# Kernel optimization log

Measured on AMD Instinct MI355X. Metric: run time of the kernel, lower is better.

The kernel has to match this reference:

```python
import jax, jax.numpy as jnp
import numpy as np

B, H, W, C = 8, 64, 64, 512
SCALING = 8
C_ = C // SCALING  # 64
N = H * W          # 4096


def setup_inputs() -> dict:
    key = jax.random.key(0)
    ks = jax.random.split(key, 8)
    scale = 1.0 / np.sqrt(C)
    x = jax.random.normal(ks[0], (B, H, W, C), dtype=jnp.float32)
    # 1x1 convs == per-pixel dense layers: weight [C_in, C_out] + bias
    Wg = jax.random.normal(ks[1], (C, C_), dtype=jnp.float32) * scale
    bg = jnp.zeros((C_,), dtype=jnp.float32)
    Wf = jax.random.normal(ks[2], (C, C_), dtype=jnp.float32) * scale
    bf = jnp.zeros((C_,), dtype=jnp.float32)
    Wh = jax.random.normal(ks[3], (C, C), dtype=jnp.float32) * scale
    bh = jnp.zeros((C,), dtype=jnp.float32)
    gamma = jnp.zeros((C,), dtype=jnp.float32)  # tf.initializers.Zeros
    return {"x": x, "Wg": Wg, "bg": bg, "Wf": Wf, "bf": bf,
            "Wh": Wh, "bh": bh, "gamma": gamma}


def reference(x, Wg, bg, Wf, bf, Wh, bh, gamma):
    b = x.shape[0]
    xf_flat = x.reshape(b, N, C)                     # [B, N, C]
    x_g = xf_flat @ Wg + bg                          # [B, N, C_]
    x_f = xf_flat @ Wf + bf                          # [B, N, C_]
    x_h = xf_flat @ Wh + bh                          # [B, N, C]
    s = jnp.einsum('bnc,bmc->bnm', x_g, x_f)         # [B, N, N]
    s = jax.nn.softmax(s, axis=-1)
    o = jnp.einsum('bnm,bmc->bnc', s, x_h)           # [B, N, C]
    o = o.reshape(b, H, W, C)
    return gamma * o + x
```

## Files before the change

### kernel.cpp

```cpp
#include <hip/hip_runtime.h>
#include <stdint.h>

using s8v  = __attribute__((ext_vector_type(8))) short;
using f4   = __attribute__((ext_vector_type(4))) float;
using u32x4 = __attribute__((ext_vector_type(4))) uint32_t;
using u32x2 = __attribute__((ext_vector_type(2))) uint32_t;
using vf4  = __attribute__((ext_vector_type(4))) float;
using i4v  = __attribute__((ext_vector_type(4))) int;

typedef unsigned short ushortT;

#define LOG2E 1.4426950408889634f

static __device__ __forceinline__ uint32_t bfr16(float f) {
  union { float f; uint32_t u; } v; v.f = f;
  return (v.u + 0x7FFFu + ((v.u >> 16) & 1u)) >> 16;
}
static __device__ __forceinline__ uint32_t pk2(float lo, float hi) {
  return (bfr16(hi) << 16) | (bfr16(lo) & 0xFFFFu);
}
static __device__ __forceinline__ uint32_t pk4fp8(float a, float b, float cc, float d) {
  int w = __builtin_amdgcn_cvt_pk_fp8_f32(a, b, 0, false);
  w = __builtin_amdgcn_cvt_pk_fp8_f32(cc, d, w, true);
  return (uint32_t)w;
}
static __device__ __forceinline__ float ex2(float x) {
#if __has_builtin(__builtin_amdgcn_exp2f)
  return __builtin_amdgcn_exp2f(x);
#else
  float r; asm("v_exp_f32 %0, %1" : "=v"(r) : "v"(x)); return r;
#endif
}
static __device__ __forceinline__ void gl16(const void* g, void* l) {
  __builtin_amdgcn_global_load_lds((const __attribute__((address_space(1))) uint32_t*)g,
                                   (__attribute__((address_space(3))) uint32_t*)l, 16, 0, 0);
}

#define MFMA_BF16(A, B, C) __builtin_amdgcn_mfma_f32_16x16x32_bf16((A), (B), (C), 0, 0, 0)
#define MFMA_FP8(A, B, C)  __builtin_amdgcn_mfma_f32_16x16x32_fp8_fp8((A), (B), (C), 0, 0, 0)

__global__ __launch_bounds__(64) void kprep(const float* __restrict__ Wg,
                                            const float* __restrict__ Wf,
                                            const float* __restrict__ Wh,
                                            ushortT* __restrict__ Wt) {
  const int cIdx = blockIdx.x;
  const int t = threadIdx.x;
  const float* src; int co, ldc;
  if (cIdx < 64)       { src = Wg; co = cIdx;       ldc = 64;  }
  else if (cIdx < 128) { src = Wf; co = cIdx - 64;  ldc = 64;  }
  else                 { src = Wh; co = cIdx - 128; ldc = 512; }
#pragma unroll
  for (int kk = 0; kk < 8; ++kk) {
    int k = kk * 64 + t;
    Wt[(size_t)cIdx * 512 + k] = (ushortT)bfr16(src[(size_t)k * ldc + co]);
  }
}

__global__ __launch_bounds__(256) void kproj(const float* __restrict__ x,
                                             const ushortT* __restrict__ Wt,
                                             const float* __restrict__ bg,
                                             const float* __restrict__ bfv,
                                             const float* __restrict__ bh,
                                             ushortT* __restrict__ Q,
                                             ushortT* __restrict__ K,
                                             uint8_t* __restrict__ V8) {
  __shared__ ushortT Al[128 * 64];
  __shared__ ushortT Bl[128 * 64];

  const int tid = threadIdx.x;
  const int w = tid >> 6, l = tid & 63, h = l >> 4, c = l & 15;
  const int wr = w >> 1, wc = w & 1;
  const int ct = blockIdx.x, rt = blockIdx.y;
  const int row0 = rt * 128;

  f4 acc[4][4];
#pragma unroll
  for (int m = 0; m < 4; ++m)
#pragma unroll
    for (int n = 0; n < 4; ++n) acc[m][n] = (f4){0.f, 0.f, 0.f, 0.f};

  const int arow = tid >> 1, ahalf = tid & 1;
  const float* xrow = x + (size_t)(row0 + arow) * 512 + ahalf * 32;
  const int asw = arow & 7;

  for (int kk = 0; kk < 8; ++kk) {
    const int k0 = kk * 64;
    vf4 f[8];
#pragma unroll
    for (int i = 0; i < 8; ++i) f[i] = *(const vf4*)(xrow + k0 + i * 4);
#pragma unroll
    for (int j = 0; j < 4; ++j) {
      u32x4 ch = { pk2(f[2*j][0], f[2*j][1]),   pk2(f[2*j][2], f[2*j][3]),
                   pk2(f[2*j+1][0], f[2*j+1][1]), pk2(f[2*j+1][2], f[2*j+1][3]) };
      *(u32x4*)((char*)Al + arow * 128 + (((ahalf * 4 + j) ^ asw) * 16)) = ch;
    }
#pragma unroll
    for (int i = 0; i < 4; ++i) {
      const int col = w * 32 + i * 8 + (l >> 3);
      const ushortT* src = Wt + (size_t)(ct * 128 + col) * 512 + k0 +
                           8 * ((l & 7) ^ (l >> 3));
      gl16(src, (char*)Bl + (w * 4 + i) * 1024);
    }
    __syncthreads();
#pragma unroll
    for (int ks = 0; ks < 2; ++ks) {
      s8v a[4], b[4];
#pragma unroll
      for (int m = 0; m < 4; ++m)
        a[m] = *(const s8v*)((char*)Al + (size_t)(wr * 64 + m * 16 + c) * 128 +
                             (((ks * 4 + h) ^ (c & 7)) * 16));
#pragma unroll
      for (int n = 0; n < 4; ++n)
        b[n] = *(const s8v*)((char*)Bl + (size_t)(wc * 64 + n * 16 + c) * 128 +
                             (((ks * 4 + h) ^ (c & 7)) * 16));
#pragma unroll
      for (int m = 0; m < 4; ++m)
#pragma unroll
        for (int n = 0; n < 4; ++n)
          acc[m][n] = MFMA_BF16(a[m], b[n], acc[m][n]);
    }
    __syncthreads();
  }

  if (ct == 0) {
    ushortT* dst = (wc == 0) ? Q : K;
    const float* bias = (wc == 0) ? bg : bfv;
    const float scl = (wc == 0) ? LOG2E : 1.0f;
#pragma unroll
    for (int n = 0; n < 4; ++n) {
      const int col = n * 16 + c;
      const float bv = bias[col];
#pragma unroll
      for (int m = 0; m < 4; ++m) {
        const int grow = row0 + wr * 64 + m * 16 + h * 4;
#pragma unroll
        for (int r = 0; r < 4; ++r)
          dst[(size_t)(grow + r) * 64 + col] = (ushortT)bfr16((acc[m][n][r] + bv) * scl);
      }
    }
  } else {
    const int b = row0 >> 12;
#pragma unroll
    for (int n = 0; n < 4; ++n) {
      const int vcol = ct * 128 + wc * 64 + n * 16 + c - 128;
      const float bv = bh[vcol];
#pragma unroll
      for (int m = 0; m < 4; ++m) {
        const int n0 = (row0 & 4095) + wr * 64 + m * 16 + h * 4;
        const int tt = n0 >> 5, kvo = n0 & 31;
        const uint32_t dd = pk4fp8(acc[m][n][0] + bv, acc[m][n][1] + bv,
                                   acc[m][n][2] + bv, acc[m][n][3] + bv);
        *(uint32_t*)(V8 + (((size_t)(b * 128 + tt) * 512 + vcol) * 32 + kvo)) = dd;
      }
    }
  }
}

__global__ __launch_bounds__(512, 4) void kattn(const ushortT* __restrict__ Qg,
                                                const ushortT* __restrict__ Kg,
                                                const uint8_t* __restrict__ V8,
                                                const float* __restrict__ x,
                                                const float* __restrict__ gamma,
                                                float* __restrict__ out) {
  __shared__ __align__(16) uint32_t Pl[2][2][512];
  __shared__ __align__(16) ushortT Klds[2][64 * 64];
  __shared__ __align__(16) float alpha_s[2][64];
  __shared__ __align__(16) int   flag_s[2][4];
  __shared__ __align__(16) float lsum_s[64];

  const int tid = threadIdx.x;
  const int w = tid >> 6, l = tid & 63, h = l >> 4, c = l & 15;
  const int bb = blockIdx.x & 7, qb = blockIdx.x >> 3;
  const size_t qrow0 = (size_t)bb * 4096 + (size_t)qb * 64;

  f4 acc[4][4];
#pragma unroll
  for (int qi = 0; qi < 4; ++qi)
#pragma unroll
    for (int vj = 0; vj < 4; ++vj) acc[qi][vj] = (f4){0.f, 0.f, 0.f, 0.f};

  const ushortT* Kb = Kg + (size_t)bb * 4096 * 64;
  const uint8_t* Vb = V8 + (size_t)bb * 512 * 4096;

  const uint8_t* vptr = Vb + (size_t)(w * 64 + c) * 32 + h * 8;
  const size_t koff = (size_t)((w & 3) * 16 + (l >> 3)) * 64 +
                      8 * ((l & 7) ^ (l >> 3));

  s8v qf[2];
  if (w < 4) {
#pragma unroll
    for (int ks = 0; ks < 2; ++ks)
      qf[ks] = *(const s8v*)(Qg + (qrow0 + w * 16 + c) * 64 + ks * 32 + h * 8);
  }
  float m_run = -__builtin_inff();
  float l_run = 0.0f;

  auto softmax_store = [&](const f4* sc, int nb) {
    float tm = fmaxf(fmaxf(fmaxf(sc[0][0], sc[0][1]), fmaxf(sc[0][2], sc[0][3])),
                     fmaxf(fmaxf(sc[1][0], sc[1][1]), fmaxf(sc[1][2], sc[1][3])));
    tm = fmaxf(tm, fmaxf(fmaxf(fmaxf(sc[2][0], sc[2][1]), fmaxf(sc[2][2], sc[2][3])),
                         fmaxf(fmaxf(sc[3][0], sc[3][1]), fmaxf(sc[3][2], sc[3][3]))));
    const unsigned long long bal = __ballot(tm > m_run + 5.77f);
    float al = 1.0f;
    if (bal) {
      tm = fmaxf(tm, __shfl_xor(tm, 16));
      tm = fmaxf(tm, __shfl_xor(tm, 32));
      const float mn = fmaxf(m_run, tm);
      al = ex2(m_run - mn);
      m_run = mn;
    }
    float ps = 0.0f;
#pragma unroll
    for (int j = 0; j < 4; ++j) {
      const float p0 = ex2(sc[j][0] - m_run), p1 = ex2(sc[j][1] - m_run);
      const float p2 = ex2(sc[j][2] - m_run), p3 = ex2(sc[j][3] - m_run);
      ps += (p0 + p1) + (p2 + p3);
      const uint32_t pw = pk4fp8(p0, p1, p2, p3);
      const int s = j >> 1;
      const int hc = 2 * (j & 1) + (h >> 1);
      Pl[nb][s][(w * 64 + c + 16 * hc) * 2 + (h & 1)] = pw;
    }
    l_run = l_run * al + ps;
    if (bal && h == 0) alpha_s[nb][w * 16 + c] = al;
    if (l == 0) flag_s[nb][w] = bal ? 1 : 0;
  };

  auto produce_lds = [&](int kb, int nb) {
    f4 sc[4];
#pragma unroll
    for (int j = 0; j < 4; ++j) sc[j] = (f4){0.f, 0.f, 0.f, 0.f};
    const char* kbp = (const char*)Klds[kb];
    __builtin_amdgcn_s_setprio(1);
#pragma unroll
    for (int j = 0; j < 4; ++j) {
#pragma unroll
      for (int ks = 0; ks < 2; ++ks) {
        s8v kf = *(const s8v*)(kbp + (size_t)(j * 16 + c) * 128 +
                               (((ks * 4 + h) ^ (c & 7)) * 16));
        sc[j] = MFMA_BF16(kf, qf[ks], sc[j]);
      }
    }
    __builtin_amdgcn_s_setprio(0);
    softmax_store(sc, nb);
  };

  if (w < 4) {
    f4 sc[4];
#pragma unroll
    for (int j = 0; j < 4; ++j) sc[j] = (f4){0.f, 0.f, 0.f, 0.f};
#pragma unroll
    for (int j = 0; j < 4; ++j) {
#pragma unroll
      for (int ks = 0; ks < 2; ++ks) {
        s8v kf = *(const s8v*)(Kb + (size_t)(j * 16 + c) * 64 + ks * 32 + h * 8);
        sc[j] = MFMA_BF16(kf, qf[ks], sc[j]);
      }
    }
    softmax_store(sc, 0);
  } else {
    gl16(Kb + 4096 + koff, (char*)Klds[1] + (w & 3) * 2048);
    gl16(Kb + 4096 + koff + 512, (char*)Klds[1] + (w & 3) * 2048 + 1024);
  }
  asm volatile("s_waitcnt vmcnt(0) lgkmcnt(0)" ::: "memory");
  __builtin_amdgcn_s_barrier();

  for (int t = 0; t < 64; ++t) {
    const int cur = t & 1;
    long paA[4], paB[4];
#pragma unroll
    for (int qi = 0; qi < 4; ++qi) {
      paA[qi] = *(const long*)&Pl[cur][0][(qi * 64 + l) * 2];
      paB[qi] = *(const long*)&Pl[cur][1][(qi * 64 + l) * 2];
    }
    i4v fl = *(const i4v*)&flag_s[cur][0];
    if (w >= 4 && t < 62) {
      const ushortT* ks_src = Kb + (size_t)(t + 2) * 4096 + koff;
      gl16(ks_src, (char*)Klds[cur] + (w & 3) * 2048);
      gl16(ks_src + 512, (char*)Klds[cur] + (w & 3) * 2048 + 1024);
    }
#pragma unroll
    for (int qi = 0; qi < 4; ++qi) {
      if (fl[qi]) {
        f4 a4 = *(const f4*)&alpha_s[cur][qi * 16 + h * 4];
#pragma unroll
        for (int vj = 0; vj < 4; ++vj)
#pragma unroll
          for (int r = 0; r < 4; ++r) acc[qi][vj][r] *= a4[r];
      }
    }
#pragma unroll
    for (int vj = 0; vj < 4; ++vj) {
      const long vf0 = *(const long*)(vptr + vj * 512);
      const long vf1 = *(const long*)(vptr + 16384 + vj * 512);
      __builtin_amdgcn_s_setprio(1);
#pragma unroll
      for (int qi = 0; qi < 4; ++qi) {
        acc[qi][vj] = MFMA_FP8(paA[qi], vf0, acc[qi][vj]);
        acc[qi][vj] = MFMA_FP8(paB[qi], vf1, acc[qi][vj]);
      }
      __builtin_amdgcn_s_setprio(0);
    }
    vptr += 32768;
    if (t < 63) {
      if (w < 4) produce_lds(cur ^ 1, cur ^ 1);
      asm volatile("s_waitcnt vmcnt(0) lgkmcnt(0)" ::: "memory");
      __builtin_amdgcn_s_barrier();
    }
  }

  l_run += __shfl_xor(l_run, 16);
  l_run += __shfl_xor(l_run, 32);
  if (w < 4 && h == 0) lsum_s[w * 16 + c] = l_run;
  __syncthreads();
#pragma unroll
  for (int qi = 0; qi < 4; ++qi) {
    f4 l4 = *(const f4*)(&lsum_s[qi * 16 + h * 4]);
    f4 rl;
#pragma unroll
    for (int r = 0; r < 4; ++r) rl[r] = 1.0f / l4[r];
#pragma unroll
    for (int vj = 0; vj < 4; ++vj) {
      const int colg = w * 64 + vj * 16 + c;
      const float gm = gamma[colg];
#pragma unroll
      for (int r = 0; r < 4; ++r) {
        const size_t idx = (qrow0 + qi * 16 + h * 4 + r) * 512 + colg;
        out[idx] = gm * (acc[qi][vj][r] * rl[r]) + x[idx];
      }
    }
  }
}

extern "C" void kernel_launch(void* const* d_in, const int* in_sizes, int n_in,
                              void* d_out, int out_size, void* d_ws, size_t ws_size,
                              hipStream_t stream) {
  const float* x     = (const float*)d_in[0];
  const float* Wg    = (const float*)d_in[1];
  const float* bg    = (const float*)d_in[2];
  const float* Wf    = (const float*)d_in[3];
  const float* bfv   = (const float*)d_in[4];
  const float* Wh    = (const float*)d_in[5];
  const float* bh    = (const float*)d_in[6];
  const float* gamma = (const float*)d_in[7];
  float* out = (float*)d_out;
  char* ws = (char*)d_ws;

  ushortT* Q  = (ushortT*)(ws);
  ushortT* K  = (ushortT*)(ws + ((size_t)4 << 20));
  uint8_t* V8 = (uint8_t*)(ws + ((size_t)8 << 20));
  ushortT* Wt = (ushortT*)(ws + ((size_t)40 << 20));

  kprep<<<dim3(640), dim3(64), 0, stream>>>(Wg, Wf, Wh, Wt);
  kproj<<<dim3(5, 256), dim3(256), 0, stream>>>(x, Wt, bg, bfv, bh, Q, K, V8);
  kattn<<<dim3(512), dim3(512), 0, stream>>>(Q, K, V8, x, gamma, out);
}
```

Measured before the change: 235.8 us.

## Use MX-scaled 16x16x128 fp8 MFMA with 128-key tiles and bf16 pre-converted x

The attention loop now handles 128 keys per step, so there are half as many barriers and pipeline stages. The P·V product uses the scaled f8f6f4 16x16x128 MFMA with unit scales in place of pairs of 16x16x32 fp8 MFMAs, with P and V laid out to feed 32-byte fragments. A separate kernel converts x to bf16 once, storing it in the output buffer as scratch, so the projection kernel can fill shared memory with direct global-to-LDS loads. The costs are an extra kernel launch with its own memory pass, doubled K LDS buffers, and higher register pressure in the attention kernel.

```diff
diff --git a/kernel.cpp b/kernel.cpp
--- a/kernel.cpp
+++ b/kernel.cpp
@@ -3,6 +3,7 @@
 
 using s8v  = __attribute__((ext_vector_type(8))) short;
 using f4   = __attribute__((ext_vector_type(4))) float;
+using i8v  = __attribute__((ext_vector_type(8))) int;
 using u32x4 = __attribute__((ext_vector_type(4))) uint32_t;
 using u32x2 = __attribute__((ext_vector_type(2))) uint32_t;
 using vf4  = __attribute__((ext_vector_type(4))) float;
@@ -37,7 +38,24 @@
 }
 
 #define MFMA_BF16(A, B, C) __builtin_amdgcn_mfma_f32_16x16x32_bf16((A), (B), (C), 0, 0, 0)
-#define MFMA_FP8(A, B, C)  __builtin_amdgcn_mfma_f32_16x16x32_fp8_fp8((A), (B), (C), 0, 0, 0)
+#define MFMA_MX(A, B, C) \
+  __builtin_amdgcn_mfma_scale_f32_16x16x128_f8f6f4((A), (B), (C), 0, 0, \
+                                                   0, 0x7F7F7F7F, 0, 0x7F7F7F7F)
+
+__global__ __launch_bounds__(256) void kxcvt(const float* __restrict__ x,
+                                             ushortT* __restrict__ xb) {
+  const size_t stride = (size_t)2048 * 256 * 8;
+  size_t idx = ((size_t)blockIdx.x * 256 + threadIdx.x) * 8;
+#pragma unroll
+  for (int i = 0; i < 4; ++i) {
+    vf4 a = *(const vf4*)(x + idx);
+    vf4 b = *(const vf4*)(x + idx + 4);
+    u32x4 o = { pk2(a[0], a[1]), pk2(a[2], a[3]),
+                pk2(b[0], b[1]), pk2(b[2], b[3]) };
+    *(u32x4*)(xb + idx) = o;
+    idx += stride;
+  }
+}
 
 __global__ __launch_bounds__(64) void kprep(const float* __restrict__ Wg,
                                             const float* __restrict__ Wf,
@@ -56,7 +74,7 @@
   }
 }
 
-__global__ __launch_bounds__(256) void kproj(const float* __restrict__ x,
+__global__ __launch_bounds__(256) void kproj(const ushortT* __restrict__ xb,
                                              const ushortT* __restrict__ Wt,
                                              const float* __restrict__ bg,
                                              const float* __restrict__ bfv,
@@ -79,20 +97,15 @@
 #pragma unroll
     for (int n = 0; n < 4; ++n) acc[m][n] = (f4){0.f, 0.f, 0.f, 0.f};
 
-  const int arow = tid >> 1, ahalf = tid & 1;
-  const float* xrow = x + (size_t)(row0 + arow) * 512 + ahalf * 32;
-  const int asw = arow & 7;
-
   for (int kk = 0; kk < 8; ++kk) {
     const int k0 = kk * 64;
-    vf4 f[8];
-#pragma unroll
-    for (int i = 0; i < 8; ++i) f[i] = *(const vf4*)(xrow + k0 + i * 4);
-#pragma unroll
-    for (int j = 0; j < 4; ++j) {
-      u32x4 ch = { pk2(f[2*j][0], f[2*j][1]),   pk2(f[2*j][2], f[2*j][3]),
-                   pk2(f[2*j+1][0], f[2*j+1][1]), pk2(f[2*j+1][2], f[2*j+1][3]) };
-      *(u32x4*)((char*)Al + arow * 128 + (((ahalf * 4 + j) ^ asw) * 16)) = ch;
+#pragma unroll
+    for (int i = 0; i < 4; ++i) {
+      const int ch = i * 256 + tid;
+      const int row = ch >> 3, kc = ch & 7;
+      const ushortT* src = xb + (size_t)(row0 + row) * 512 + k0 +
+                           8 * (kc ^ (row & 7));
+      gl16(src, (char*)Al + ch * 16);
     }
 #pragma unroll
     for (int i = 0; i < 4; ++i) {
@@ -162,8 +175,8 @@
                                                 const float* __restrict__ x,
                                                 const float* __restrict__ gamma,
                                                 float* __restrict__ out) {
-  __shared__ __align__(16) uint32_t Pl[2][2][512];
-  __shared__ __align__(16) ushortT Klds[2][64 * 64];
+  __shared__ __align__(16) uint32_t Pl[2][2048];
+  __shared__ __align__(16) ushortT Klds[2][2][64 * 64];
   __shared__ __align__(16) float alpha_s[2][64];
   __shared__ __align__(16) int   flag_s[2][4];
   __shared__ __align__(16) float lsum_s[64];
@@ -182,7 +195,7 @@
   const ushortT* Kb = Kg + (size_t)bb * 4096 * 64;
   const uint8_t* Vb = V8 + (size_t)bb * 512 * 4096;
 
-  const uint8_t* vptr = Vb + (size_t)(w * 64 + c) * 32 + h * 8;
+  const uint8_t* vptr = Vb + (size_t)h * 16384 + (size_t)(w * 64 + c) * 32;
   const size_t koff = (size_t)((w & 3) * 16 + (l >> 3)) * 64 +
                       8 * ((l & 7) ^ (l >> 3));
 
@@ -195,11 +208,12 @@
   float m_run = -__builtin_inff();
   float l_run = 0.0f;
 
-  auto softmax_store = [&](const f4* sc, int nb) {
-    float tm = fmaxf(fmaxf(fmaxf(sc[0][0], sc[0][1]), fmaxf(sc[0][2], sc[0][3])),
-                     fmaxf(fmaxf(sc[1][0], sc[1][1]), fmaxf(sc[1][2], sc[1][3])));
-    tm = fmaxf(tm, fmaxf(fmaxf(fmaxf(sc[2][0], sc[2][1]), fmaxf(sc[2][2], sc[2][3])),
-                         fmaxf(fmaxf(sc[3][0], sc[3][1]), fmaxf(sc[3][2], sc[3][3]))));
+  auto softmax_store8 = [&](const f4* sc, int nb) {
+    float tm = sc[0][0];
+#pragma unroll
+    for (int idx = 0; idx < 8; ++idx)
+#pragma unroll
+      for (int r = 0; r < 4; ++r) tm = fmaxf(tm, sc[idx][r]);
     const unsigned long long bal = __ballot(tm > m_run + 5.77f);
     float al = 1.0f;
     if (bal) {
@@ -211,72 +225,80 @@
     }
     float ps = 0.0f;
 #pragma unroll
-    for (int j = 0; j < 4; ++j) {
-      const float p0 = ex2(sc[j][0] - m_run), p1 = ex2(sc[j][1] - m_run);
-      const float p2 = ex2(sc[j][2] - m_run), p3 = ex2(sc[j][3] - m_run);
-      ps += (p0 + p1) + (p2 + p3);
-      const uint32_t pw = pk4fp8(p0, p1, p2, p3);
-      const int s = j >> 1;
-      const int hc = 2 * (j & 1) + (h >> 1);
-      Pl[nb][s][(w * 64 + c + 16 * hc) * 2 + (h & 1)] = pw;
-    }
+    for (int T = 0; T < 2; ++T)
+#pragma unroll
+      for (int j = 0; j < 4; ++j) {
+        const int idx = T * 4 + j;
+        const float p0 = ex2(sc[idx][0] - m_run), p1 = ex2(sc[idx][1] - m_run);
+        const float p2 = ex2(sc[idx][2] - m_run), p3 = ex2(sc[idx][3] - m_run);
+        ps += (p0 + p1) + (p2 + p3);
+        const uint32_t pw = pk4fp8(p0, p1, p2, p3);
+        Pl[nb][(w * 64 + c + 16 * (2 * T + (j >> 1))) * 8 + 4 * (j & 1) + h] = pw;
+      }
     l_run = l_run * al + ps;
     if (bal && h == 0) alpha_s[nb][w * 16 + c] = al;
     if (l == 0) flag_s[nb][w] = bal ? 1 : 0;
   };
 
   auto produce_lds = [&](int kb, int nb) {
-    f4 sc[4];
-#pragma unroll
-    for (int j = 0; j < 4; ++j) sc[j] = (f4){0.f, 0.f, 0.f, 0.f};
-    const char* kbp = (const char*)Klds[kb];
+    f4 sc[8];
+#pragma unroll
+    for (int i = 0; i < 8; ++i) sc[i] = (f4){0.f, 0.f, 0.f, 0.f};
     __builtin_amdgcn_s_setprio(1);
 #pragma unroll
-    for (int j = 0; j < 4; ++j) {
-#pragma unroll
-      for (int ks = 0; ks < 2; ++ks) {
-        s8v kf = *(const s8v*)(kbp + (size_t)(j * 16 + c) * 128 +
-                               (((ks * 4 + h) ^ (c & 7)) * 16));
-        sc[j] = MFMA_BF16(kf, qf[ks], sc[j]);
-      }
+    for (int T = 0; T < 2; ++T) {
+      const char* kbp = (const char*)Klds[kb][T];
+#pragma unroll
+      for (int j = 0; j < 4; ++j)
+#pragma unroll
+        for (int ks = 0; ks < 2; ++ks) {
+          s8v kf = *(const s8v*)(kbp + (size_t)(j * 16 + c) * 128 +
+                                 (((ks * 4 + h) ^ (c & 7)) * 16));
+          sc[T * 4 + j] = MFMA_BF16(kf, qf[ks], sc[T * 4 + j]);
+        }
     }
     __builtin_amdgcn_s_setprio(0);
-    softmax_store(sc, nb);
+    softmax_store8(sc, nb);
   };
 
   if (w < 4) {
-    f4 sc[4];
-#pragma unroll
-    for (int j = 0; j < 4; ++j) sc[j] = (f4){0.f, 0.f, 0.f, 0.f};
-#pragma unroll
-    for (int j = 0; j < 4; ++j) {
-#pragma unroll
-      for (int ks = 0; ks < 2; ++ks) {
-        s8v kf = *(const s8v*)(Kb + (size_t)(j * 16 + c) * 64 + ks * 32 + h * 8);
-        sc[j] = MFMA_BF16(kf, qf[ks], sc[j]);
-      }
-    }
-    softmax_store(sc, 0);
+    f4 sc[8];
+#pragma unroll
+    for (int i = 0; i < 8; ++i) sc[i] = (f4){0.f, 0.f, 0.f, 0.f};
+#pragma unroll
+    for (int T = 0; T < 2; ++T)
+#pragma unroll
+      for (int j = 0; j < 4; ++j)
+#pragma unroll
+        for (int ks = 0; ks < 2; ++ks) {
+          s8v kf = *(const s8v*)(Kb + (size_t)(T * 64 + j * 16 + c) * 64 +
+                                 ks * 32 + h * 8);
+          sc[T * 4 + j] = MFMA_BF16(kf, qf[ks], sc[T * 4 + j]);
+        }
+    softmax_store8(sc, 0);
   } else {
-    gl16(Kb + 4096 + koff, (char*)Klds[1] + (w & 3) * 2048);
-    gl16(Kb + 4096 + koff + 512, (char*)Klds[1] + (w & 3) * 2048 + 1024);
+    const ushortT* ksrc = Kb + 8192 + koff;
+    gl16(ksrc,              (char*)Klds[1][0] + (w & 3) * 2048);
+    gl16(ksrc + 512,        (char*)Klds[1][0] + (w & 3) * 2048 + 1024);
+    gl16(ksrc + 4096,       (char*)Klds[1][1] + (w & 3) * 2048);
+    gl16(ksrc + 4096 + 512, (char*)Klds[1][1] + (w & 3) * 2048 + 1024);
   }
   asm volatile("s_waitcnt vmcnt(0) lgkmcnt(0)" ::: "memory");
   __builtin_amdgcn_s_barrier();
 
-  for (int t = 0; t < 64; ++t) {
-    const int cur = t & 1;
-    long paA[4], paB[4];
-#pragma unroll
-    for (int qi = 0; qi < 4; ++qi) {
-      paA[qi] = *(const long*)&Pl[cur][0][(qi * 64 + l) * 2];
-      paB[qi] = *(const long*)&Pl[cur][1][(qi * 64 + l) * 2];
-    }
+  for (int e = 0; e < 32; ++e) {
+    const int cur = e & 1;
+    i8v pa[4];
+#pragma unroll
+    for (int qi = 0; qi < 4; ++qi)
+      pa[qi] = *(const i8v*)&Pl[cur][(qi * 64 + l) * 8];
     i4v fl = *(const i4v*)&flag_s[cur][0];
-    if (w >= 4 && t < 62) {
-      const ushortT* ks_src = Kb + (size_t)(t + 2) * 4096 + koff;
-      gl16(ks_src, (char*)Klds[cur] + (w & 3) * 2048);
-      gl16(ks_src + 512, (char*)Klds[cur] + (w & 3) * 2048 + 1024);
+    if (w >= 4 && e < 30) {
+      const ushortT* ksrc = Kb + (size_t)(e + 2) * 8192 + koff;
+      gl16(ksrc,              (char*)Klds[cur][0] + (w & 3) * 2048);
+      gl16(ksrc + 512,        (char*)Klds[cur][0] + (w & 3) * 2048 + 1024);
+      gl16(ksrc + 4096,       (char*)Klds[cur][1] + (w & 3) * 2048);
+      gl16(ksrc + 4096 + 512, (char*)Klds[cur][1] + (w & 3) * 2048 + 1024);
     }
 #pragma unroll
     for (int qi = 0; qi < 4; ++qi) {
@@ -290,19 +312,16 @@
     }
 #pragma unroll
     for (int vj = 0; vj < 4; ++vj) {
-      const long vf0 = *(const long*)(vptr + vj * 512);
-      const long vf1 = *(const long*)(vptr + 16384 + vj * 512);
+      const i8v vf = *(const i8v*)(vptr + vj * 512);
       __builtin_amdgcn_s_setprio(1);
 #pragma unroll
-      for (int qi = 0; qi < 4; ++qi) {
-        acc[qi][vj] = MFMA_FP8(paA[qi], vf0, acc[qi][vj]);
-        acc[qi][vj] = MFMA_FP8(paB[qi], vf1, acc[qi][vj]);
-      }
+      for (int qi = 0; qi < 4; ++qi)
+        acc[qi][vj] = MFMA_MX(pa[qi], vf, acc[qi][vj]);
       __builtin_amdgcn_s_setprio(0);
     }
-    vptr += 32768;
-    if (t < 63) {
-      if (w < 4) produce_lds(cur ^ 1, cur ^ 1);
+    vptr += 65536;
+    if (w < 4 && e < 31) produce_lds(cur ^ 1, cur ^ 1);
+    if (e < 31) {
       asm volatile("s_waitcnt vmcnt(0) lgkmcnt(0)" ::: "memory");
       __builtin_amdgcn_s_barrier();
     }
@@ -349,8 +368,10 @@
   ushortT* K  = (ushortT*)(ws + ((size_t)4 << 20));
   uint8_t* V8 = (uint8_t*)(ws + ((size_t)8 << 20));
   ushortT* Wt = (ushortT*)(ws + ((size_t)40 << 20));
-
+  ushortT* xb = (ushortT*)d_out;
+
+  kxcvt<<<dim3(2048), dim3(256), 0, stream>>>(x, xb);
   kprep<<<dim3(640), dim3(64), 0, stream>>>(Wg, Wf, Wh, Wt);
-  kproj<<<dim3(5, 256), dim3(256), 0, stream>>>(x, Wt, bg, bfv, bh, Q, K, V8);
+  kproj<<<dim3(5, 256), dim3(256), 0, stream>>>(xb, Wt, bg, bfv, bh, Q, K, V8);
   kattn<<<dim3(512), dim3(512), 0, stream>>>(Q, K, V8, x, gamma, out);
 }
```

Result: slower. 436.9 us (+85.3%).
